# Performance work log

Hardware: AMD Instinct MI355X
Metric: run time of the kernel (lower is better)

The kernel has to match this reference:

```python
import jax, jax.numpy as jnp
import numpy as np

IN_DIM = 3
OUT_DIM = 3
HSI_DIM = 31
MIN_BAND = 400.0
MAX_BAND = 700.0
N_BAND = 31  # == HSI_DIM so the indexed write fills every column
BN_EPS = 1e-5


def setup_inputs() -> dict:
    key = jax.random.key(0)
    ks = jax.random.split(key, 8)
    B, H, W = 16, 256, 256
    x = jax.random.uniform(ks[0], (B, H, W, IN_DIM), jnp.float32)
    x_hsi = jax.random.uniform(ks[1], (B, H, W, HSI_DIM), jnp.float32)
    conv_w = jax.random.normal(ks[2], (64, IN_DIM, 3, 3), jnp.float32) * 0.1
    conv_b = jax.random.normal(ks[3], (64,), jnp.float32) * 0.1
    bn_w = 1.0 + jax.random.normal(ks[4], (64,), jnp.float32) * 0.1
    bn_b = jax.random.normal(ks[5], (64,), jnp.float32) * 0.1
    fc_w = jax.random.normal(ks[6], (OUT_DIM + 2, 64), jnp.float32) * 0.1
    fc_b = jax.random.normal(ks[7], (OUT_DIM + 2,), jnp.float32) * 0.1
    return {"x": x, "x_hsi": x_hsi, "conv_w": conv_w, "conv_b": conv_b,
            "bn_w": bn_w, "bn_b": bn_b, "fc_w": fc_w, "fc_b": fc_b}


def _voltage_net(x, conv_w, conv_b, bn_w, bn_b, fc_w, fc_b):
    # x: (B, H, W, 3) channels-last -> NCHW
    xp = jnp.transpose(x, (0, 3, 1, 2))
    y = jax.lax.conv_general_dilated(
        xp, conv_w, window_strides=(1, 1), padding='SAME',
        dimension_numbers=('NCHW', 'OIHW', 'NCHW')) + conv_b[None, :, None, None]
    # BatchNorm2d (training-mode batch statistics, biased variance)
    mu = y.mean(axis=(0, 2, 3))
    var = y.var(axis=(0, 2, 3))
    y = (y - mu[None, :, None, None]) * jax.lax.rsqrt(var + BN_EPS)[None, :, None, None]
    y = y * bn_w[None, :, None, None] + bn_b[None, :, None, None]
    y = jax.nn.relu(y)
    feat = y.mean(axis=(2, 3))                      # AdaptiveAvgPool2d(1) -> (B, 64)
    raw = feat @ fc_w.T + fc_b                      # (B, out_dim + 2)
    mn = raw.min(axis=1, keepdims=True)
    mx = raw.max(axis=1, keepdims=True)
    norm = (raw - mn) / (mx - mn + 1e-8)
    mid = jnp.sort(norm, axis=1)[:, 1:-1]           # drop smallest & largest
    return mid * 10.0                               # (B, out_dim) voltages


def reference(x, x_hsi, conv_w, conv_b, bn_w, bn_b, fc_w, fc_b):
    voltages = _voltage_net(x, conv_w, conv_b, bn_w, bn_b, fc_w, fc_b)  # (B, C)
    # Vectorized Lyot SRF (replaces per-batch python loop); nBand == hsi_dim
    n = jnp.arange(N_BAND, dtype=jnp.float32)
    band = MIN_BAND + (MAX_BAND - MIN_BAND) * n / N_BAND                # (A,)
    cos_part = jnp.cos(2.0 * jnp.pi * (-0.01) / voltages)               # (B, C)
    srf = (0.5 - 0.5 * cos_part)[:, :, None] / (band[None, None, :] * 1e-6)  # (B, C, A)
    # contract hyperspectral bands: (B,C,A) x (B,H,W,A) -> (B,H,W,C)
    return jnp.einsum('bca,bpqa->bpqc', srf, x_hsi)
```

## Files before the change

kernel.cpp:

```cpp
#include <hip/hip_runtime.h>
#include <hip/hip_bf16.h>
#include <math.h>

#define BB 16
#define HH 256
#define WW 256

#define OFF_CHSUM 0
#define OFF_CHSQ  64
#define OFF_FEAT  256
#define OFF_Z     2048

#define SM_PAN   0
#define SM_W     21728
#define SM_B     28640
#define SM_RED   28896
#define SM_G     31744
#define SM_BYTES 32000

typedef __attribute__((ext_vector_type(8))) short bf16x8;
typedef __attribute__((ext_vector_type(4))) float f32x4;

union BFu { __hip_bfloat16 h; short s; };
union ABu { bf16x8 v; unsigned u[4]; };

__device__ __forceinline__ unsigned packsplit(float v) {
    BFu hi; hi.h = __float2bfloat16(v);
    float rs = v - __bfloat162float(hi.h);
    BFu lo; lo.h = __float2bfloat16(rs);
    return (unsigned)(unsigned short)hi.s | ((unsigned)(unsigned short)lo.s << 16);
}

__global__ void k_init(float* __restrict__ ws) {
    int i = blockIdx.x * 256 + threadIdx.x;
    if (i < 1280) ws[i] = 0.f;
}

template <int MODE>
__global__ __launch_bounds__(256) void k_convz(const float* __restrict__ x,
                                               const float* __restrict__ xh,
                                               const float* __restrict__ cw,
                                               const float* __restrict__ cb,
                                               const float* __restrict__ bnw,
                                               const float* __restrict__ bnb,
                                               float* __restrict__ ws) {
    __shared__ __align__(16) char smem[SM_BYTES];
    const int t = threadIdx.x;
    const int b = blockIdx.y;

    if (blockIdx.x >= 64) {
        float* s_x = (float*)smem;
        float* s_g = (float*)(smem + SM_G);
        const int zx = blockIdx.x - 64;
        if (t < 31) {
            const float band = 400.f + (300.f * (float)t) / 31.f;
            s_g[t] = 1.f / (band * 1e-6f);
        }
#pragma unroll 1
        for (int c = 0; c < 8; ++c) {
            const size_t pxbase = (size_t)b * 65536 + zx * 2048 + c * 256;
            const float4* xg = (const float4*)(xh + pxbase * 31);
            float4* sx4 = (float4*)s_x;
#pragma unroll
            for (int i = 0; i < 8; ++i) {
                int idx = t + (i << 8);
                if (idx < 1984) sx4[idx] = xg[idx];
            }
            __syncthreads();
            float z = 0.f;
            const float* px = s_x + t * 31;
#pragma unroll
            for (int a = 0; a < 31; ++a) z = fmaf(px[a], s_g[a], z);
            ws[OFF_Z + pxbase + t] = z;
            __syncthreads();
        }
        return;
    }

    unsigned* pan32 = (unsigned*)smem;
    float* s_w = (float*)(smem + SM_W);
    float* s_b = (float*)(smem + SM_B);
    float (*red)[4][16][2] = (float (*)[4][16][2])(smem + SM_RED);

    const int lane = t & 63;
    const int wv   = t >> 6;
    const int r0   = blockIdx.x * 4;
    const int mrow = lane & 15;
    const int s    = lane >> 4;
    const bool s3  = (s == 3);
    const float* __restrict__ xb = x + (size_t)b * (HH * WW * 3);

    for (int i = t; i < 1728; i += 256) s_w[i] = cw[i];
    if (t < 64) s_b[t] = cb[t];

    for (int e = t; e < 6 * 774; e += 256) {
        const int l = e / 774, j = e - l * 774;
        const int gr = r0 - 1 + l, gcf = j - 3;
        const bool ok = ((unsigned)gr < 256u) && ((unsigned)gcf < 768u);
        int off = gr * 768 + gcf;
        off = ok ? off : 0;
        float v = xb[off];
        v = ok ? v : 0.f;
        pan32[l * 776 + j] = packsplit(v);
    }
    for (int j = t; j < 776; j += 256) pan32[6 * 776 + j] = 0x3F80u;

    float av[4], bvv[4];
#pragma unroll
    for (int n = 0; n < 4; ++n) {
        const int ch = n * 16 + mrow;
        if (MODE == 1) {
            const float invN = 1.f / 1048576.f;
            const float mu = ws[OFF_CHSUM + ch] * invN;
            const float vr = ws[OFF_CHSQ + ch] * invN - mu * mu;
            const float rs = rsqrtf(vr + 1e-5f);
            av[n]  = rs * bnw[ch];
            bvv[n] = bnb[ch] - mu * av[n];
        } else { av[n] = 1.f; bvv[n] = 0.f; }
    }

    int off8[8];
#pragma unroll
    for (int e = 0; e < 8; ++e) {
        if (!s3)        off8[e] = (wv + s) * 776 + e;
        else if (e < 3) off8[e] = (wv + e) * 776 + 8;
        else            off8[e] = 6 * 776 + e;
    }
    const int mrow3 = mrow * 3;

    __syncthreads();

    bf16x8 bh[4], bl[4];
#pragma unroll
    for (int n = 0; n < 4; ++n) {
        const int ch = n * 16 + mrow;
#pragma unroll
        for (int e = 0; e < 8; ++e) {
            float w = 0.f;
            if (!s3) {
                w = s_w[ch * 27 + (e % 3) * 9 + s * 3 + (e / 3)];
            } else if (e < 3) {
                w = s_w[ch * 27 + 18 + e * 3 + 2];
            } else if (e == 3) {
                w = s_b[ch];
            }
            if (MODE == 1) {
                w *= av[n];
                if (s3 && e == 3) w += bvv[n];
            }
            BFu hi; hi.h = __float2bfloat16(w);
            const float rs2 = w - __bfloat162float(hi.h);
            BFu lo; lo.h = __float2bfloat16(rs2);
            bh[n][e] = hi.s;
            bl[n][e] = lo.s;
        }
    }

    float a0[4] = {0.f, 0.f, 0.f, 0.f};
    float a1[4] = {0.f, 0.f, 0.f, 0.f};

#define GATHER(W, CS)                                                   \
    {                                                                   \
        const int c3 = (CS) * 48 + mrow3;                               \
        W[0] = pan32[off8[0] + c3]; W[1] = pan32[off8[1] + c3];         \
        W[2] = pan32[off8[2] + c3]; W[3] = pan32[off8[3] + c3];         \
        W[4] = pan32[off8[4] + c3]; W[5] = pan32[off8[5] + c3];         \
        W[6] = pan32[off8[6] + c3]; W[7] = pan32[off8[7] + c3];         \
    }
#define COMPUTE(W)                                                      \
    {                                                                   \
        ABu ua, ul;                                                     \
        ua.u[0] = __builtin_amdgcn_perm(W[1], W[0], 0x05040100u);       \
        ua.u[1] = __builtin_amdgcn_perm(W[3], W[2], 0x05040100u);       \
        ua.u[2] = __builtin_amdgcn_perm(W[5], W[4], 0x05040100u);       \
        ua.u[3] = __builtin_amdgcn_perm(W[7], W[6], 0x05040100u);       \
        ul.u[0] = __builtin_amdgcn_perm(W[1], W[0], 0x07060302u);       \
        ul.u[1] = __builtin_amdgcn_perm(W[3], W[2], 0x07060302u);       \
        ul.u[2] = __builtin_amdgcn_perm(W[5], W[4], 0x07060302u);       \
        ul.u[3] = __builtin_amdgcn_perm(W[7], W[6], 0x07060302u);       \
        const bf16x8 ah = ua.v, al = ul.v;                              \
        __builtin_amdgcn_s_setprio(1);                                  \
        _Pragma("unroll")                                               \
        for (int n = 0; n < 4; ++n) {                                   \
            f32x4 acc = {0.f, 0.f, 0.f, 0.f};                           \
            acc = __builtin_amdgcn_mfma_f32_16x16x32_bf16(ah, bl[n], acc, 0, 0, 0); \
            acc = __builtin_amdgcn_mfma_f32_16x16x32_bf16(al, bh[n], acc, 0, 0, 0); \
            acc = __builtin_amdgcn_mfma_f32_16x16x32_bf16(ah, bh[n], acc, 0, 0, 0); \
            _Pragma("unroll")                                           \
            for (int i = 0; i < 4; ++i) {                               \
                const float y = acc[i];                                 \
                if (MODE == 0) { a0[n] += y; a1[n] = fmaf(y, y, a1[n]); } \
                else { a0[n] += fmaxf(y, 0.f); }                        \
            }                                                           \
        }                                                               \
        __builtin_amdgcn_s_setprio(0);                                  \
    }

    {
        unsigned Wa[8], Wb[8];
        GATHER(Wa, 0)
        GATHER(Wb, 1)  COMPUTE(Wa)
        GATHER(Wa, 2)  COMPUTE(Wb)
        GATHER(Wb, 3)  COMPUTE(Wa)
        GATHER(Wa, 4)  COMPUTE(Wb)
        GATHER(Wb, 5)  COMPUTE(Wa)
        GATHER(Wa, 6)  COMPUTE(Wb)
        GATHER(Wb, 7)  COMPUTE(Wa)
        GATHER(Wa, 8)  COMPUTE(Wb)
        GATHER(Wb, 9)  COMPUTE(Wa)
        GATHER(Wa, 10) COMPUTE(Wb)
        GATHER(Wb, 11) COMPUTE(Wa)
        GATHER(Wa, 12) COMPUTE(Wb)
        GATHER(Wb, 13) COMPUTE(Wa)
        GATHER(Wa, 14) COMPUTE(Wb)
        GATHER(Wb, 15) COMPUTE(Wa)
        COMPUTE(Wb)
    }
#undef GATHER
#undef COMPUTE

#pragma unroll
    for (int n = 0; n < 4; ++n) {
        a0[n] += __shfl_xor(a0[n], 16);
        a0[n] += __shfl_xor(a0[n], 32);
        if (MODE == 0) {
            a1[n] += __shfl_xor(a1[n], 16);
            a1[n] += __shfl_xor(a1[n], 32);
        }
    }
    if (lane < 16) {
#pragma unroll
        for (int n = 0; n < 4; ++n) {
            red[wv][n][lane][0] = a0[n];
            red[wv][n][lane][1] = (MODE == 0) ? a1[n] : 0.f;
        }
    }
    __syncthreads();
    if (t < 64) {
        const int n = t >> 4, m = t & 15;
        const float S = red[0][n][m][0] + red[1][n][m][0] + red[2][n][m][0] + red[3][n][m][0];
        if (MODE == 0) {
            const float Q = red[0][n][m][1] + red[1][n][m][1] + red[2][n][m][1] + red[3][n][m][1];
            atomicAdd(&ws[OFF_CHSUM + t], S);
            atomicAdd(&ws[OFF_CHSQ + t], Q);
        } else {
            atomicAdd(&ws[OFF_FEAT + b * 64 + t], S);
        }
    }
}

__global__ __launch_bounds__(256) void k_final2(const float* __restrict__ fcw,
                                                const float* __restrict__ fcb,
                                                const float* __restrict__ ws,
                                                float* __restrict__ out) {
    __shared__ float s_raw[5];
    __shared__ float sp[3];
    __shared__ float s_o[768];
    const int t = threadIdx.x;
    const int blk = blockIdx.x;
    const int b = blk >> 8;
    const size_t pix0 = (size_t)blk << 8;

    if (t < 5) {
        const float inv = 1.f / 65536.f;
        float a = fcb[t];
        for (int c = 0; c < 64; ++c)
            a = fmaf(fcw[t * 64 + c], ws[OFF_FEAT + b * 64 + c] * inv, a);
        s_raw[t] = a;
    }
    __syncthreads();
    if (t == 0) {
        float raw[5];
#pragma unroll
        for (int j = 0; j < 5; ++j) raw[j] = s_raw[j];
#define CS(i, j)                              \
        {                                     \
            float lo = fminf(raw[i], raw[j]); \
            float hi = fmaxf(raw[i], raw[j]); \
            raw[i] = lo;                      \
            raw[j] = hi;                      \
        }
        CS(0, 1) CS(3, 4) CS(2, 4) CS(2, 3) CS(0, 3) CS(0, 2) CS(1, 4) CS(1, 3) CS(1, 2)
#undef CS
        const float mn = raw[0], mx = raw[4];
        const float sc = 10.f / (mx - mn + 1e-8f);
#pragma unroll
        for (int c2 = 0; c2 < 3; ++c2) {
            const float v = (raw[1 + c2] - mn) * sc;
            const float sh = sinf(0.031415926535897934f / v);
            sp[c2] = sh * sh;
        }
    }
    __syncthreads();
    const float z = ws[OFF_Z + pix0 + t];
    s_o[t * 3 + 0] = sp[0] * z;
    s_o[t * 3 + 1] = sp[1] * z;
    s_o[t * 3 + 2] = sp[2] * z;
    __syncthreads();
    float* ob = out + pix0 * 3;
#pragma unroll
    for (int i = 0; i < 3; ++i) ob[t + (i << 8)] = s_o[t + (i << 8)];
}

extern "C" void kernel_launch(void* const* d_in, const int* in_sizes, int n_in,
                              void* d_out, int out_size, void* d_ws, size_t ws_size,
                              hipStream_t stream) {
    const float* x    = (const float*)d_in[0];
    const float* xhsi = (const float*)d_in[1];
    const float* cw   = (const float*)d_in[2];
    const float* cb   = (const float*)d_in[3];
    const float* bnw  = (const float*)d_in[4];
    const float* bnb  = (const float*)d_in[5];
    const float* fcw  = (const float*)d_in[6];
    const float* fcb  = (const float*)d_in[7];
    float* out = (float*)d_out;
    float* ws  = (float*)d_ws;

    hipLaunchKernelGGL(k_init, dim3(5), dim3(256), 0, stream, ws);
    hipLaunchKernelGGL((k_convz<0>), dim3(96, 16), dim3(256), 0, stream,
                       x, xhsi, cw, cb, bnw, bnb, ws);
    hipLaunchKernelGGL((k_convz<1>), dim3(64, 16), dim3(256), 0, stream,
                       x, xhsi, cw, cb, bnw, bnb, ws);
    hipLaunchKernelGGL(k_final2, dim3(4096), dim3(256), 0, stream, fcw, fcb, ws, out);
}
```

Measured before the change: 83.73 us.

## Double conv block size to 512 threads, splitting column strips across wave halves

The conv/statistics kernel now launches 512 threads per block. Each of 8 waves handles one of 4 rows and half of the 768 packed columns, so each wave runs 8 gather/compute steps instead of 16. The reduction buffer is enlarged to 8 wave slots. In the hyperspectral contraction blocks only half the threads compute while all threads help load. The aim is more waves in flight and a shorter per-wave serial chain, at the cost of tighter register limits from launch_bounds(512,8) and idle threads in the z blocks.

```diff
diff --git a/kernel.cpp b/kernel.cpp
--- a/kernel.cpp
+++ b/kernel.cpp
@@ -16,7 +16,7 @@
 #define SM_B     28640
 #define SM_RED   28896
 #define SM_G     31744
-#define SM_BYTES 32000
+#define SM_BYTES 32992
 
 typedef __attribute__((ext_vector_type(8))) short bf16x8;
 typedef __attribute__((ext_vector_type(4))) float f32x4;
@@ -37,13 +37,13 @@
 }
 
 template <int MODE>
-__global__ __launch_bounds__(256) void k_convz(const float* __restrict__ x,
-                                               const float* __restrict__ xh,
-                                               const float* __restrict__ cw,
-                                               const float* __restrict__ cb,
-                                               const float* __restrict__ bnw,
-                                               const float* __restrict__ bnb,
-                                               float* __restrict__ ws) {
+__global__ __launch_bounds__(512, 8) void k_convz(const float* __restrict__ x,
+                                                  const float* __restrict__ xh,
+                                                  const float* __restrict__ cw,
+                                                  const float* __restrict__ cb,
+                                                  const float* __restrict__ bnw,
+                                                  const float* __restrict__ bnb,
+                                                  float* __restrict__ ws) {
     __shared__ __align__(16) char smem[SM_BYTES];
     const int t = threadIdx.x;
     const int b = blockIdx.y;
@@ -61,17 +61,15 @@
             const size_t pxbase = (size_t)b * 65536 + zx * 2048 + c * 256;
             const float4* xg = (const float4*)(xh + pxbase * 31);
             float4* sx4 = (float4*)s_x;
-#pragma unroll
-            for (int i = 0; i < 8; ++i) {
-                int idx = t + (i << 8);
-                if (idx < 1984) sx4[idx] = xg[idx];
+            for (int i = t; i < 1984; i += 512) sx4[i] = xg[i];
+            __syncthreads();
+            if (t < 256) {
+                float z = 0.f;
+                const float* px = s_x + t * 31;
+#pragma unroll
+                for (int a = 0; a < 31; ++a) z = fmaf(px[a], s_g[a], z);
+                ws[OFF_Z + pxbase + t] = z;
             }
-            __syncthreads();
-            float z = 0.f;
-            const float* px = s_x + t * 31;
-#pragma unroll
-            for (int a = 0; a < 31; ++a) z = fmaf(px[a], s_g[a], z);
-            ws[OFF_Z + pxbase + t] = z;
             __syncthreads();
         }
         return;
@@ -83,17 +81,19 @@
     float (*red)[4][16][2] = (float (*)[4][16][2])(smem + SM_RED);
 
     const int lane = t & 63;
-    const int wv   = t >> 6;
+    const int w8   = t >> 6;
+    const int rr   = w8 & 3;
+    const int half = w8 >> 2;
     const int r0   = blockIdx.x * 4;
     const int mrow = lane & 15;
     const int s    = lane >> 4;
     const bool s3  = (s == 3);
     const float* __restrict__ xb = x + (size_t)b * (HH * WW * 3);
 
-    for (int i = t; i < 1728; i += 256) s_w[i] = cw[i];
+    for (int i = t; i < 1728; i += 512) s_w[i] = cw[i];
     if (t < 64) s_b[t] = cb[t];
 
-    for (int e = t; e < 6 * 774; e += 256) {
+    for (int e = t; e < 6 * 774; e += 512) {
         const int l = e / 774, j = e - l * 774;
         const int gr = r0 - 1 + l, gcf = j - 3;
         const bool ok = ((unsigned)gr < 256u) && ((unsigned)gcf < 768u);
@@ -103,7 +103,7 @@
         v = ok ? v : 0.f;
         pan32[l * 776 + j] = packsplit(v);
     }
-    for (int j = t; j < 776; j += 256) pan32[6 * 776 + j] = 0x3F80u;
+    for (int j = t; j < 776; j += 512) pan32[6 * 776 + j] = 0x3F80u;
 
     float av[4], bvv[4];
 #pragma unroll
@@ -122,11 +122,11 @@
     int off8[8];
 #pragma unroll
     for (int e = 0; e < 8; ++e) {
-        if (!s3)        off8[e] = (wv + s) * 776 + e;
-        else if (e < 3) off8[e] = (wv + e) * 776 + 8;
+        if (!s3)        off8[e] = (rr + s) * 776 + e;
+        else if (e < 3) off8[e] = (rr + e) * 776 + 8;
         else            off8[e] = 6 * 776 + e;
     }
-    const int mrow3 = mrow * 3;
+    const int cbase = half * 384 + mrow * 3;
 
     __syncthreads();
 
@@ -161,7 +161,7 @@
 
 #define GATHER(W, CS)                                                   \
     {                                                                   \
-        const int c3 = (CS) * 48 + mrow3;                               \
+        const int c3 = cbase + (CS) * 48;                               \
         W[0] = pan32[off8[0] + c3]; W[1] = pan32[off8[1] + c3];         \
         W[2] = pan32[off8[2] + c3]; W[3] = pan32[off8[3] + c3];         \
         W[4] = pan32[off8[4] + c3]; W[5] = pan32[off8[5] + c3];         \
@@ -206,14 +206,6 @@
         GATHER(Wb, 5)  COMPUTE(Wa)
         GATHER(Wa, 6)  COMPUTE(Wb)
         GATHER(Wb, 7)  COMPUTE(Wa)
-        GATHER(Wa, 8)  COMPUTE(Wb)
-        GATHER(Wb, 9)  COMPUTE(Wa)
-        GATHER(Wa, 10) COMPUTE(Wb)
-        GATHER(Wb, 11) COMPUTE(Wa)
-        GATHER(Wa, 12) COMPUTE(Wb)
-        GATHER(Wb, 13) COMPUTE(Wa)
-        GATHER(Wa, 14) COMPUTE(Wb)
-        GATHER(Wb, 15) COMPUTE(Wa)
         COMPUTE(Wb)
     }
 #undef GATHER
@@ -231,16 +223,20 @@
     if (lane < 16) {
 #pragma unroll
         for (int n = 0; n < 4; ++n) {
-            red[wv][n][lane][0] = a0[n];
-            red[wv][n][lane][1] = (MODE == 0) ? a1[n] : 0.f;
+            red[w8][n][lane][0] = a0[n];
+            red[w8][n][lane][1] = (MODE == 0) ? a1[n] : 0.f;
         }
     }
     __syncthreads();
     if (t < 64) {
         const int n = t >> 4, m = t & 15;
-        const float S = red[0][n][m][0] + red[1][n][m][0] + red[2][n][m][0] + red[3][n][m][0];
+        float S = 0.f, Q = 0.f;
+#pragma unroll
+        for (int w = 0; w < 8; ++w) {
+            S += red[w][n][m][0];
+            if (MODE == 0) Q += red[w][n][m][1];
+        }
         if (MODE == 0) {
-            const float Q = red[0][n][m][1] + red[1][n][m][1] + red[2][n][m][1] + red[3][n][m][1];
             atomicAdd(&ws[OFF_CHSUM + t], S);
             atomicAdd(&ws[OFF_CHSQ + t], Q);
         } else {
@@ -317,9 +313,9 @@
     float* ws  = (float*)d_ws;
 
     hipLaunchKernelGGL(k_init, dim3(5), dim3(256), 0, stream, ws);
-    hipLaunchKernelGGL((k_convz<0>), dim3(96, 16), dim3(256), 0, stream,
+    hipLaunchKernelGGL((k_convz<0>), dim3(96, 16), dim3(512), 0, stream,
                        x, xhsi, cw, cb, bnw, bnb, ws);
-    hipLaunchKernelGGL((k_convz<1>), dim3(64, 16), dim3(256), 0, stream,
+    hipLaunchKernelGGL((k_convz<1>), dim3(64, 16), dim3(512), 0, stream,
                        x, xhsi, cw, cb, bnw, bnb, ws);
     hipLaunchKernelGGL(k_final2, dim3(4096), dim3(256), 0, stream, fcw, fcb, ws, out);
 }
```

New measurement: 152.3 us. 1.82x slower.
